# Kernel optimization log

Measured on AMD Instinct MI355X. Metric: run time of the kernel, lower is better.

The kernel has to match this reference:

```python
import jax, jax.numpy as jnp
import numpy as np

# TuckerLinear: in_features = out_features = 4096, num_modes = 3
IN_SHAPE = (16, 16, 16)    # get_shape(4096, 3)
OUT_SHAPE = (16, 16, 16)
IN_FEATURES = 4096
OUT_FEATURES = 4096


def setup_inputs() -> dict:
    key = jax.random.key(0)
    ks = jax.random.split(key, 12)
    B, S = 4, 4096
    x = jax.random.normal(ks[0], (B, S, IN_FEATURES), dtype=jnp.float32)
    core = jax.random.normal(ks[1], (8, 8, 8, 8, 8, 8), dtype=jnp.float32) * 0.05
    fi0 = jax.random.normal(ks[2], (16, 8), dtype=jnp.float32) * 0.3
    fi1 = jax.random.normal(ks[3], (16, 8), dtype=jnp.float32) * 0.3
    fi2 = jax.random.normal(ks[4], (16, 8), dtype=jnp.float32) * 0.3
    fo0 = jax.random.normal(ks[5], (16, 8), dtype=jnp.float32) * 0.3
    fo1 = jax.random.normal(ks[6], (16, 8), dtype=jnp.float32) * 0.3
    fo2 = jax.random.normal(ks[7], (16, 8), dtype=jnp.float32) * 0.3
    bias = jax.random.normal(ks[8], (OUT_FEATURES,), dtype=jnp.float32) * 0.01
    per_dim_scale = jnp.ones((OUT_FEATURES,), dtype=jnp.float32)
    alpha = jnp.ones((1,), dtype=jnp.float32)
    input_perm = jax.random.permutation(ks[9], IN_FEATURES).astype(jnp.int32)
    return dict(x=x, core=core, fi0=fi0, fi1=fi1, fi2=fi2,
                fo0=fo0, fo1=fo1, fo2=fo2,
                per_dim_scale=per_dim_scale, alpha=alpha, bias=bias,
                input_perm=input_perm)


def reference(x, core, fi0, fi1, fi2, fo0, fo1, fo2,
              per_dim_scale, alpha, bias, input_perm):
    batch_dims = x.shape[:-1]
    # 1. input channel permutation (spectral reordering)
    xp = jnp.take(x, input_perm, axis=-1)
    # 2. reshape to expose input modes: (N, 16, 16, 16)
    t = xp.reshape(-1, *IN_SHAPE)
    # 3. contract each input mode with its factor (16 -> 8)
    t = jnp.einsum('nabc,ap->npbc', t, fi0)
    t = jnp.einsum('npbc,bq->npqc', t, fi1)
    t = jnp.einsum('npqc,cr->npqr', t, fi2)
    # 4. contract with core over all input-rank modes: (N,8,8,8) -> (N,8,8,8)
    t = jnp.einsum('npqr,xyzpqr->nxyz', t, core)
    # 5. contract each output mode with its factor (8 -> 16)
    t = jnp.einsum('nxyz,Xx->nXyz', t, fo0)
    t = jnp.einsum('nXyz,Yy->nXYz', t, fo1)
    t = jnp.einsum('nXYz,Zz->nXYZ', t, fo2)
    # 6. flatten output modes, scale, bias
    out = t.reshape(-1, OUT_FEATURES)
    out = out * per_dim_scale * alpha + bias
    return out.reshape(*batch_dims, OUT_FEATURES)
```

## Files before the change

kernel.cpp:

```cpp
#include <hip/hip_runtime.h>
#include <stdint.h>

#define NROWS 16384
#define D 4096

typedef __bf16 bf16x8 __attribute__((ext_vector_type(8)));
typedef float  f32x4  __attribute__((ext_vector_type(4)));

__device__ inline unsigned short f2bf(float f) {
    unsigned u = __float_as_uint(f);
    u += 0x7fffu + ((u >> 16) & 1u);
    return (unsigned short)(u >> 16);
}

__global__ __launch_bounds__(256) void k_corebf(const float* __restrict__ core,
                                                unsigned int* __restrict__ cb) {
    const int o = blockIdx.x;
    const int kp = threadIdx.x;
    float2 v = *(const float2*)&core[o * 512 + 2 * kp];
    cb[((size_t)(kp >> 2) * 512 + o) * 4 + (kp & 3)] =
        (unsigned)f2bf(v.x) | ((unsigned)f2bf(v.y) << 16);
}

__global__ __launch_bounds__(256, 3) void k_t3(const float* __restrict__ x,
                                               const float* __restrict__ fi0,
                                               const float* __restrict__ fi1,
                                               const float* __restrict__ fi2,
                                               const int* __restrict__ perm,
                                               unsigned int* __restrict__ t3out) {
    __shared__ float xr[2][4096];
    __shared__ float t1[2048];
    __shared__ float t2[1024];
    __shared__ float fac[3][128];

    const int tid = threadIdx.x;
    const int n0 = blockIdx.x * 4;

    {
        const int h = tid & 127;
        fac[0][h] = fi0[h];
        fac[1][h] = fi1[h];
        fac[2][h] = fi2[h];
    }
    int pj[16];
    #pragma unroll
    for (int j = 0; j < 16; ++j) pj[j] = perm[j * 256 + tid];

    auto stage = [&](int b, int row) {
        const float4* src = (const float4*)(x + (size_t)row * D);
        #pragma unroll
        for (int i = 0; i < 4; ++i) {
            const int c = i * 256 + tid;
            __builtin_amdgcn_global_load_lds(
                (const __attribute__((address_space(1))) void*)(src + c),
                (__attribute__((address_space(3))) void*)(&xr[b][c * 4]),
                16, 0, 0);
        }
    };

    auto STEP3 = [&](int b) {
        float a8[8] = {0,0,0,0,0,0,0,0};
        #pragma unroll
        for (int a = 0; a < 16; ++a) {
            float v = xr[b][pj[a]];
            #pragma unroll
            for (int p = 0; p < 8; ++p) a8[p] += v * fac[0][a * 8 + p];
        }
        #pragma unroll
        for (int p = 0; p < 8; ++p) t1[p * 256 + tid] = a8[p];
    };
    auto STEP4 = [&]() {
        const int p = tid >> 5, c = (tid >> 1) & 15, qh = tid & 1;
        float a4[4] = {0,0,0,0};
        #pragma unroll
        for (int b = 0; b < 16; ++b) {
            float v = t1[p * 256 + b * 16 + c];
            #pragma unroll
            for (int qi = 0; qi < 4; ++qi) a4[qi] += v * fac[1][b * 8 + qh * 4 + qi];
        }
        #pragma unroll
        for (int qi = 0; qi < 4; ++qi) t2[p * 128 + (qh * 4 + qi) * 16 + c] = a4[qi];
    };
    auto STEP5_PACK = [&](int n) {
        const int p = tid >> 5, q = (tid >> 2) & 7, rh = tid & 3;
        float a2[2] = {0,0};
        #pragma unroll
        for (int c = 0; c < 16; ++c) {
            float v = t2[p * 128 + q * 16 + c];
            #pragma unroll
            for (int ri = 0; ri < 2; ++ri) a2[ri] += v * fac[2][c * 8 + rh * 2 + ri];
        }
        const int kt = tid >> 5, k4 = (tid >> 2) & 7, w = tid & 3;
        t3out[(((size_t)kt * 8 + k4) * NROWS + n) * 4 + w] =
            (unsigned)f2bf(a2[0]) | ((unsigned)f2bf(a2[1]) << 16);
    };

    stage(0, n0 + 0);
    stage(1, n0 + 1);

    asm volatile("s_waitcnt vmcnt(4) lgkmcnt(0)" ::: "memory");
    __builtin_amdgcn_s_barrier();
    STEP3(0);
    asm volatile("s_waitcnt lgkmcnt(0)" ::: "memory");
    __builtin_amdgcn_s_barrier();
    stage(0, n0 + 2);
    STEP4();
    asm volatile("s_waitcnt lgkmcnt(0)" ::: "memory");
    __builtin_amdgcn_s_barrier();
    STEP5_PACK(n0 + 0);

    asm volatile("s_waitcnt vmcnt(5)" ::: "memory");
    __builtin_amdgcn_s_barrier();
    STEP3(1);
    asm volatile("s_waitcnt lgkmcnt(0)" ::: "memory");
    __builtin_amdgcn_s_barrier();
    stage(1, n0 + 3);
    STEP4();
    asm volatile("s_waitcnt lgkmcnt(0)" ::: "memory");
    __builtin_amdgcn_s_barrier();
    STEP5_PACK(n0 + 1);

    asm volatile("s_waitcnt vmcnt(6)" ::: "memory");
    __builtin_amdgcn_s_barrier();
    STEP3(0);
    asm volatile("s_waitcnt lgkmcnt(0)" ::: "memory");
    __builtin_amdgcn_s_barrier();
    STEP4();
    asm volatile("s_waitcnt lgkmcnt(0)" ::: "memory");
    __builtin_amdgcn_s_barrier();
    STEP5_PACK(n0 + 2);

    asm volatile("s_waitcnt vmcnt(2)" ::: "memory");
    __builtin_amdgcn_s_barrier();
    STEP3(1);
    asm volatile("s_waitcnt lgkmcnt(0)" ::: "memory");
    __builtin_amdgcn_s_barrier();
    STEP4();
    asm volatile("s_waitcnt lgkmcnt(0)" ::: "memory");
    __builtin_amdgcn_s_barrier();
    STEP5_PACK(n0 + 3);
}

__global__ __launch_bounds__(256, 2) void k_core(const __bf16* __restrict__ t3,
                                                 const __bf16* __restrict__ cb,
                                                 unsigned short* __restrict__ t4) {
    __shared__ __bf16 lA[2][8192];
    __shared__ __bf16 lB[2][8192];

    const int tid = threadIdx.x, lane = tid & 63, wv = tid >> 6;

    const int bid = blockIdx.x;
    const int wgid = (bid & 7) * 64 + (bid >> 3);
    const int m0 = (wgid >> 2) * 128;
    const int n0 = (wgid & 3) * 128;
    const int wm = wv >> 1, wn = wv & 1;
    const int l15 = lane & 15, l4 = lane >> 4;

    auto stage = [&](int b, int kt) {
        #pragma unroll
        for (int i = 0; i < 4; ++i) {
            const int c = i * 256 + tid;
            const int k4 = c >> 7, r = c & 127;
            const __bf16* ga = t3 + ((size_t)(kt * 8 + k4) * NROWS + m0 + r) * 8;
            __builtin_amdgcn_global_load_lds(
                (const __attribute__((address_space(1))) void*)ga,
                (__attribute__((address_space(3))) void*)(&lA[b][(size_t)c * 8]),
                16, 0, 0);
            const __bf16* gb = cb + ((size_t)(kt * 8 + k4) * 512 + n0 + r) * 8;
            __builtin_amdgcn_global_load_lds(
                (const __attribute__((address_space(1))) void*)gb,
                (__attribute__((address_space(3))) void*)(&lB[b][(size_t)c * 8]),
                16, 0, 0);
        }
    };

    f32x4 acc[4][4] = {};

    auto compute = [&](int cur) {
        #pragma unroll
        for (int kk = 0; kk < 2; ++kk) {
            const int k4f = kk * 4 + l4;
            bf16x8 af[4], bfr[4];
            #pragma unroll
            for (int mt = 0; mt < 4; ++mt)
                af[mt] = *(const bf16x8*)&lA[cur][(k4f * 128 + wm * 64 + mt * 16 + l15) * 8];
            #pragma unroll
            for (int nt = 0; nt < 4; ++nt)
                bfr[nt] = *(const bf16x8*)&lB[cur][(k4f * 128 + wn * 64 + nt * 16 + l15) * 8];
            #pragma unroll
            for (int mt = 0; mt < 4; ++mt)
                #pragma unroll
                for (int nt = 0; nt < 4; ++nt)
                    acc[mt][nt] = __builtin_amdgcn_mfma_f32_16x16x32_bf16(
                        af[mt], bfr[nt], acc[mt][nt], 0, 0, 0);
        }
    };

    stage(0, 0);
    stage(1, 1);
    #pragma unroll 1
    for (int kt = 0; kt < 8; ++kt) {
        if (kt < 7) asm volatile("s_waitcnt vmcnt(8)" ::: "memory");
        else        asm volatile("s_waitcnt vmcnt(0)" ::: "memory");
        __builtin_amdgcn_s_barrier();
        __builtin_amdgcn_s_setprio(1);
        compute(kt & 1);
        __builtin_amdgcn_s_setprio(0);
        __builtin_amdgcn_s_barrier();
        if (kt < 6) stage(kt & 1, kt + 2);
    }

    #pragma unroll
    for (int nt = 0; nt < 4; ++nt) {
        const int col = n0 + wn * 64 + nt * 16 + l15;
        #pragma unroll
        for (int mt = 0; mt < 4; ++mt) {
            const int row = m0 + wm * 64 + mt * 16 + l4 * 4;
            #pragma unroll
            for (int j = 0; j < 4; ++j)
                t4[(size_t)(row + j) * 512 + col] = f2bf(acc[mt][nt][j]);
        }
    }
}

__global__ __launch_bounds__(256, 2) void k_expand(const unsigned short* __restrict__ t4,
                                                   const float* __restrict__ fo0,
                                                   const float* __restrict__ fo1,
                                                   const float* __restrict__ fo2,
                                                   const float* __restrict__ pds,
                                                   const float* __restrict__ alphap,
                                                   const float* __restrict__ bias,
                                                   float* __restrict__ out) {
    __shared__ __bf16 t4L[4][2][512];
    __shared__ float  t5L[4][1024];
    __shared__ float  t6L[4][2304];
    __shared__ float  fo0L[128];

    const int tid = threadIdx.x, w = tid >> 6, l = tid & 63;
    const int n0 = blockIdx.x * 32 + w * 8;
    const int ly = l >> 3, lz = l & 7;
    const int lq = l & 3, lx = l >> 2;

    if (tid < 128) fo0L[tid] = fo0[tid];
    const float alpha = alphap[0];

    float fo1f[2][8];
    #pragma unroll
    for (int h = 0; h < 2; ++h) {
        f32x4 a = *(const f32x4*)&fo1[(h * 8 + ly) * 8];
        f32x4 b = *(const f32x4*)&fo1[(h * 8 + ly) * 8 + 4];
        #pragma unroll
        for (int j = 0; j < 4; ++j) { fo1f[h][j] = a[j]; fo1f[h][4 + j] = b[j]; }
    }
    float fo2s[4][8];
    #pragma unroll
    for (int j = 0; j < 4; ++j) {
        f32x4 a = *(const f32x4*)&fo2[(lq * 4 + j) * 8];
        f32x4 b = *(const f32x4*)&fo2[(lq * 4 + j) * 8 + 4];
        #pragma unroll
        for (int zz = 0; zz < 4; ++zz) { fo2s[j][zz] = a[zz]; fo2s[j][4 + zz] = b[zz]; }
    }

    auto stage = [&](int b, int n) {
        const unsigned short* src = t4 + (size_t)n * 512 + l * 8;
        __builtin_amdgcn_global_load_lds(
            (const __attribute__((address_space(1))) void*)src,
            (__attribute__((address_space(3))) void*)(&t4L[w][b][l * 8]),
            16, 0, 0);
    };

    stage(0, n0);
    asm volatile("s_waitcnt vmcnt(0) lgkmcnt(0)" ::: "memory");
    __syncthreads();

    #pragma unroll 1
    for (int r = 0; r < 8; ++r) {
        const int b = r & 1;
        if (r) asm volatile("s_waitcnt vmcnt(48)" ::: "memory");

        float rv[8];
        #pragma unroll
        for (int xx = 0; xx < 8; ++xx)
            rv[xx] = (float)t4L[w][b][xx * 64 + l];
        if (r + 1 < 8) stage(b ^ 1, n0 + r + 1);
        #pragma unroll
        for (int X = 0; X < 16; ++X) {
            f32x4 f0 = *(const f32x4*)&fo0L[X * 8];
            f32x4 f1 = *(const f32x4*)&fo0L[X * 8 + 4];
            float s = rv[0] * f0[0] + rv[1] * f0[1] + rv[2] * f0[2] + rv[3] * f0[3]
                    + rv[4] * f1[0] + rv[5] * f1[1] + rv[6] * f1[2] + rv[7] * f1[3];
            t5L[w][X * 64 + lz * 8 + ly] = s;
        }
        asm volatile("s_waitcnt lgkmcnt(0)" ::: "memory");

        #pragma unroll
        for (int X = 0; X < 16; ++X) {
            f32x4 u0 = *(const f32x4*)&t5L[w][X * 64 + lz * 8];
            f32x4 u1 = *(const f32x4*)&t5L[w][X * 64 + lz * 8 + 4];
            float a0 = u0[0] * fo1f[0][0] + u0[1] * fo1f[0][1] + u0[2] * fo1f[0][2] + u0[3] * fo1f[0][3]
                     + u1[0] * fo1f[0][4] + u1[1] * fo1f[0][5] + u1[2] * fo1f[0][6] + u1[3] * fo1f[0][7];
            float a1 = u0[0] * fo1f[1][0] + u0[1] * fo1f[1][1] + u0[2] * fo1f[1][2] + u0[3] * fo1f[1][3]
                     + u1[0] * fo1f[1][4] + u1[1] * fo1f[1][5] + u1[2] * fo1f[1][6] + u1[3] * fo1f[1][7];
            t6L[w][(X * 16 + ly) * 9 + lz]     = a0;
            t6L[w][(X * 16 + ly + 8) * 9 + lz] = a1;
        }
        asm volatile("s_waitcnt lgkmcnt(0)" ::: "memory");

        float* orow = out + (size_t)(n0 + r) * 4096;
        #pragma unroll
        for (int c2 = 0; c2 < 16; ++c2) {
            const int XY = c2 * 16 + lx;
            f32x4 pq = *(const f32x4*)&pds[c2 * 256 + l * 4];
            f32x4 bq = *(const f32x4*)&bias[c2 * 256 + l * 4];
            float tv[8];
            #pragma unroll
            for (int zz = 0; zz < 8; ++zz) tv[zz] = t6L[w][XY * 9 + zz];
            f32x4 o4;
            #pragma unroll
            for (int j = 0; j < 4; ++j) {
                float t7 = tv[0] * fo2s[j][0] + tv[1] * fo2s[j][1]
                         + tv[2] * fo2s[j][2] + tv[3] * fo2s[j][3]
                         + tv[4] * fo2s[j][4] + tv[5] * fo2s[j][5]
                         + tv[6] * fo2s[j][6] + tv[7] * fo2s[j][7];
                o4[j] = t7 * (pq[j] * alpha) + bq[j];
            }
            *(f32x4*)&orow[c2 * 256 + l * 4] = o4;
        }
    }
}

extern "C" void kernel_launch(void* const* d_in, const int* in_sizes, int n_in,
                              void* d_out, int out_size, void* d_ws, size_t ws_size,
                              hipStream_t stream) {
    const float* x     = (const float*)d_in[0];
    const float* core  = (const float*)d_in[1];
    const float* fi0   = (const float*)d_in[2];
    const float* fi1   = (const float*)d_in[3];
    const float* fi2   = (const float*)d_in[4];
    const float* fo0   = (const float*)d_in[5];
    const float* fo1   = (const float*)d_in[6];
    const float* fo2   = (const float*)d_in[7];
    const float* pds   = (const float*)d_in[8];
    const float* alpha = (const float*)d_in[9];
    const float* bias  = (const float*)d_in[10];
    const int*   perm  = (const int*)d_in[11];
    float* outp = (float*)d_out;

    char* ws = (char*)d_ws;
    unsigned int*   cb   = (unsigned int*)(ws);
    unsigned int*   t3ws = (unsigned int*)(ws + 1048576);
    unsigned short* t4   = (unsigned short*)(ws + 17825792);

    k_corebf<<<512, 256, 0, stream>>>(core, cb);
    k_t3<<<NROWS / 4, 256, 0, stream>>>(x, fi0, fi1, fi2, perm, t3ws);
    k_core<<<512, 256, 0, stream>>>((const __bf16*)t3ws, (const __bf16*)cb, t4);
    k_expand<<<512, 256, 0, stream>>>(t4, fo0, fo1, fo2, pds, alpha, bias, outp);
}
```

Before: 174.0 us.

## Store t4 in lane-contiguous order and load rows directly into registers

The producer kernel now writes t4 with a permuted column index so that each lane's eight x-values are contiguous. This lets the expand kernel fetch a row with one 16-byte global load per lane into registers instead of staging through LDS with global_load_lds. The LDS staging buffer is removed and occupancy is raised to 3 blocks per SM, with register double-buffering of the next rows. This trades the async LDS pipeline for plain register prefetch and adds register pressure.

Measured after the change: 269.4 us. 1.55x slower.

```diff
diff --git a/kernel.cpp b/kernel.cpp
--- a/kernel.cpp
+++ b/kernel.cpp
@@ -213,17 +213,18 @@
     #pragma unroll
     for (int nt = 0; nt < 4; ++nt) {
         const int col = n0 + wn * 64 + nt * 16 + l15;
+        const int oo = (col & 63) * 8 + (col >> 6);
         #pragma unroll
         for (int mt = 0; mt < 4; ++mt) {
             const int row = m0 + wm * 64 + mt * 16 + l4 * 4;
             #pragma unroll
             for (int j = 0; j < 4; ++j)
-                t4[(size_t)(row + j) * 512 + col] = f2bf(acc[mt][nt][j]);
-        }
-    }
-}
-
-__global__ __launch_bounds__(256, 2) void k_expand(const unsigned short* __restrict__ t4,
+                t4[(size_t)(row + j) * 512 + oo] = f2bf(acc[mt][nt][j]);
+        }
+    }
+}
+
+__global__ __launch_bounds__(256, 3) void k_expand(const unsigned short* __restrict__ t4,
                                                    const float* __restrict__ fo0,
                                                    const float* __restrict__ fo1,
                                                    const float* __restrict__ fo2,
@@ -231,7 +232,6 @@
                                                    const float* __restrict__ alphap,
                                                    const float* __restrict__ bias,
                                                    float* __restrict__ out) {
-    __shared__ __bf16 t4L[4][2][512];
     __shared__ float  t5L[4][1024];
     __shared__ float  t6L[4][2304];
     __shared__ float  fo0L[128];
@@ -261,28 +261,14 @@
         for (int zz = 0; zz < 4; ++zz) { fo2s[j][zz] = a[zz]; fo2s[j][4 + zz] = b[zz]; }
     }
 
-    auto stage = [&](int b, int n) {
-        const unsigned short* src = t4 + (size_t)n * 512 + l * 8;
-        __builtin_amdgcn_global_load_lds(
-            (const __attribute__((address_space(1))) void*)src,
-            (__attribute__((address_space(3))) void*)(&t4L[w][b][l * 8]),
-            16, 0, 0);
-    };
-
-    stage(0, n0);
-    asm volatile("s_waitcnt vmcnt(0) lgkmcnt(0)" ::: "memory");
-    __syncthreads();
-
-    #pragma unroll 1
-    for (int r = 0; r < 8; ++r) {
-        const int b = r & 1;
-        if (r) asm volatile("s_waitcnt vmcnt(48)" ::: "memory");
-
+    auto loadrow = [&](int n) -> bf16x8 {
+        return *(const bf16x8*)(t4 + (size_t)n * 512 + l * 8);
+    };
+
+    auto ROW = [&](bf16x8 vcur, int r) {
         float rv[8];
         #pragma unroll
-        for (int xx = 0; xx < 8; ++xx)
-            rv[xx] = (float)t4L[w][b][xx * 64 + l];
-        if (r + 1 < 8) stage(b ^ 1, n0 + r + 1);
+        for (int xx = 0; xx < 8; ++xx) rv[xx] = (float)vcur[xx];
         #pragma unroll
         for (int X = 0; X < 16; ++X) {
             f32x4 f0 = *(const f32x4*)&fo0L[X * 8];
@@ -326,6 +312,21 @@
             }
             *(f32x4*)&orow[c2 * 256 + l * 4] = o4;
         }
+        asm volatile("s_waitcnt lgkmcnt(0)" ::: "memory");
+    };
+
+    bf16x8 va = loadrow(n0 + 0);
+    bf16x8 vb = loadrow(n0 + 1);
+    __syncthreads();
+
+    #pragma unroll
+    for (int rr = 0; rr < 8; rr += 2) {
+        bf16x8 vc = va;
+        if (rr + 2 < 8) va = loadrow(n0 + rr + 2);
+        ROW(vc, rr);
+        bf16x8 vd = vb;
+        if (rr + 3 < 8) vb = loadrow(n0 + rr + 3);
+        ROW(vd, rr + 1);
     }
 }
 
```

## Process one row per block in k_t3 and drop the manual double-buffer pipeline

Applied to the files above, without the earlier changes.

The input-factor contraction kernel now handles a single row per workgroup instead of four, with a single LDS row buffer and no software double-buffering. The grid grows fourfold and the occupancy hint rises from 3 to 5 blocks per CU, so latency hiding comes from more resident workgroups instead of intra-block prefetch. In exchange, each block reloads the factors and the 16-entry permutation for only one row, and block launch overhead goes up.

Result: faster. 167.8 us (-3.6%).

```diff
diff --git a/kernel.cpp b/kernel.cpp
--- a/kernel.cpp
+++ b/kernel.cpp
@@ -22,19 +22,19 @@
         (unsigned)f2bf(v.x) | ((unsigned)f2bf(v.y) << 16);
 }
 
-__global__ __launch_bounds__(256, 3) void k_t3(const float* __restrict__ x,
+__global__ __launch_bounds__(256, 5) void k_t3(const float* __restrict__ x,
                                                const float* __restrict__ fi0,
                                                const float* __restrict__ fi1,
                                                const float* __restrict__ fi2,
                                                const int* __restrict__ perm,
                                                unsigned int* __restrict__ t3out) {
-    __shared__ float xr[2][4096];
+    __shared__ float xr[4096];
     __shared__ float t1[2048];
     __shared__ float t2[1024];
     __shared__ float fac[3][128];
 
     const int tid = threadIdx.x;
-    const int n0 = blockIdx.x * 4;
+    const int n = blockIdx.x;
 
     {
         const int h = tid & 127;
@@ -46,30 +46,35 @@
     #pragma unroll
     for (int j = 0; j < 16; ++j) pj[j] = perm[j * 256 + tid];
 
-    auto stage = [&](int b, int row) {
-        const float4* src = (const float4*)(x + (size_t)row * D);
+    {
+        const float4* src = (const float4*)(x + (size_t)n * D);
         #pragma unroll
         for (int i = 0; i < 4; ++i) {
             const int c = i * 256 + tid;
             __builtin_amdgcn_global_load_lds(
                 (const __attribute__((address_space(1))) void*)(src + c),
-                (__attribute__((address_space(3))) void*)(&xr[b][c * 4]),
+                (__attribute__((address_space(3))) void*)(&xr[c * 4]),
                 16, 0, 0);
         }
-    };
-
-    auto STEP3 = [&](int b) {
+    }
+    asm volatile("s_waitcnt vmcnt(0) lgkmcnt(0)" ::: "memory");
+    __builtin_amdgcn_s_barrier();
+
+    {
         float a8[8] = {0,0,0,0,0,0,0,0};
         #pragma unroll
         for (int a = 0; a < 16; ++a) {
-            float v = xr[b][pj[a]];
+            float v = xr[pj[a]];
             #pragma unroll
             for (int p = 0; p < 8; ++p) a8[p] += v * fac[0][a * 8 + p];
         }
         #pragma unroll
         for (int p = 0; p < 8; ++p) t1[p * 256 + tid] = a8[p];
-    };
-    auto STEP4 = [&]() {
+    }
+    asm volatile("s_waitcnt lgkmcnt(0)" ::: "memory");
+    __builtin_amdgcn_s_barrier();
+
+    {
         const int p = tid >> 5, c = (tid >> 1) & 15, qh = tid & 1;
         float a4[4] = {0,0,0,0};
         #pragma unroll
@@ -80,8 +85,11 @@
         }
         #pragma unroll
         for (int qi = 0; qi < 4; ++qi) t2[p * 128 + (qh * 4 + qi) * 16 + c] = a4[qi];
-    };
-    auto STEP5_PACK = [&](int n) {
+    }
+    asm volatile("s_waitcnt lgkmcnt(0)" ::: "memory");
+    __builtin_amdgcn_s_barrier();
+
+    {
         const int p = tid >> 5, q = (tid >> 2) & 7, rh = tid & 3;
         float a2[2] = {0,0};
         #pragma unroll
@@ -93,52 +101,7 @@
         const int kt = tid >> 5, k4 = (tid >> 2) & 7, w = tid & 3;
         t3out[(((size_t)kt * 8 + k4) * NROWS + n) * 4 + w] =
             (unsigned)f2bf(a2[0]) | ((unsigned)f2bf(a2[1]) << 16);
-    };
-
-    stage(0, n0 + 0);
-    stage(1, n0 + 1);
-
-    asm volatile("s_waitcnt vmcnt(4) lgkmcnt(0)" ::: "memory");
-    __builtin_amdgcn_s_barrier();
-    STEP3(0);
-    asm volatile("s_waitcnt lgkmcnt(0)" ::: "memory");
-    __builtin_amdgcn_s_barrier();
-    stage(0, n0 + 2);
-    STEP4();
-    asm volatile("s_waitcnt lgkmcnt(0)" ::: "memory");
-    __builtin_amdgcn_s_barrier();
-    STEP5_PACK(n0 + 0);
-
-    asm volatile("s_waitcnt vmcnt(5)" ::: "memory");
-    __builtin_amdgcn_s_barrier();
-    STEP3(1);
-    asm volatile("s_waitcnt lgkmcnt(0)" ::: "memory");
-    __builtin_amdgcn_s_barrier();
-    stage(1, n0 + 3);
-    STEP4();
-    asm volatile("s_waitcnt lgkmcnt(0)" ::: "memory");
-    __builtin_amdgcn_s_barrier();
-    STEP5_PACK(n0 + 1);
-
-    asm volatile("s_waitcnt vmcnt(6)" ::: "memory");
-    __builtin_amdgcn_s_barrier();
-    STEP3(0);
-    asm volatile("s_waitcnt lgkmcnt(0)" ::: "memory");
-    __builtin_amdgcn_s_barrier();
-    STEP4();
-    asm volatile("s_waitcnt lgkmcnt(0)" ::: "memory");
-    __builtin_amdgcn_s_barrier();
-    STEP5_PACK(n0 + 2);
-
-    asm volatile("s_waitcnt vmcnt(2)" ::: "memory");
-    __builtin_amdgcn_s_barrier();
-    STEP3(1);
-    asm volatile("s_waitcnt lgkmcnt(0)" ::: "memory");
-    __builtin_amdgcn_s_barrier();
-    STEP4();
-    asm volatile("s_waitcnt lgkmcnt(0)" ::: "memory");
-    __builtin_amdgcn_s_barrier();
-    STEP5_PACK(n0 + 3);
+    }
 }
 
 __global__ __launch_bounds__(256, 2) void k_core(const __bf16* __restrict__ t3,
@@ -352,7 +315,7 @@
     unsigned short* t4   = (unsigned short*)(ws + 17825792);
 
     k_corebf<<<512, 256, 0, stream>>>(core, cb);
-    k_t3<<<NROWS / 4, 256, 0, stream>>>(x, fi0, fi1, fi2, perm, t3ws);
+    k_t3<<<NROWS, 256, 0, stream>>>(x, fi0, fi1, fi2, perm, t3ws);
     k_core<<<512, 256, 0, stream>>>((const __bf16*)t3ws, (const __bf16*)cb, t4);
     k_expand<<<512, 256, 0, stream>>>(t4, fo0, fo1, fo2, pds, alpha, bias, outp);
 }
```
